# Kernel optimization log

Measured on AMD Instinct MI355X. Metric: run time of the kernel, lower is better.

Reference implementation:

```python
import jax, jax.numpy as jnp
import numpy as np

WIN = (8, 7, 7)
SHIFT = (4, 3, 3)  # window_size // 2, applied on the 2nd (shifted) block
HEADS = 24
DIM = 768
RPB_SIZE = (2 * WIN[0] - 1) * (2 * WIN[1] - 1) * (2 * WIN[2] - 1)  # 2535


def rel_pos_index():
    d, h, w = WIN
    coords = np.stack(np.meshgrid(np.arange(d), np.arange(h), np.arange(w), indexing='ij')).reshape(3, -1)
    rel = (coords[:, :, None] - coords[:, None, :]).transpose(1, 2, 0)
    rel[:, :, 0] += d - 1
    rel[:, :, 1] += h - 1
    rel[:, :, 2] += w - 1
    rel[:, :, 0] *= (2 * h - 1) * (2 * w - 1)
    rel[:, :, 1] *= 2 * w - 1
    return rel.sum(-1).astype(np.int32)


def compute_mask(D, H, W):
    # static shapes -> pure numpy, traced-constant under jit
    img = np.zeros((D, H, W), np.float32)
    cnt = 0
    sl = lambda ws, ss: [slice(None, -ws), slice(-ws, -ss), slice(-ss, None)]
    for d in sl(WIN[0], SHIFT[0]):
        for h in sl(WIN[1], SHIFT[1]):
            for w in sl(WIN[2], SHIFT[2]):
                img[d, h, w] = cnt
                cnt += 1
    m = img.reshape(D // WIN[0], WIN[0], H // WIN[1], WIN[1], W // WIN[2], WIN[2])
    m = m.transpose(0, 2, 4, 1, 3, 5).reshape(-1, WIN[0] * WIN[1] * WIN[2])
    am = m[:, None, :] - m[:, :, None]
    return jnp.asarray(np.where(am != 0, -100.0, 0.0).astype(np.float32))  # (nW, N, N)


def window_partition(x):
    B, D, H, W, C = x.shape
    x = x.reshape(B, D // WIN[0], WIN[0], H // WIN[1], WIN[1], W // WIN[2], WIN[2], C)
    return x.transpose(0, 1, 3, 5, 2, 4, 6, 7).reshape(-1, WIN[0] * WIN[1] * WIN[2], C)


def window_reverse(win, B, D, H, W):
    x = win.reshape(B, D // WIN[0], H // WIN[1], W // WIN[2], WIN[0], WIN[1], WIN[2], -1)
    return x.transpose(0, 1, 4, 2, 5, 3, 6, 7).reshape(B, D, H, W, -1)


def layer_norm(x, g, b, eps=1e-5):
    mu = x.mean(-1, keepdims=True)
    var = ((x - mu) ** 2).mean(-1, keepdims=True)
    return (x - mu) * jax.lax.rsqrt(var + eps) * g + b


def gelu(x):
    return jax.nn.gelu(x, approximate=False)  # torch nn.GELU default = exact erf


def window_attention(xw, p, rpi, mask):
    Bw, N, C = xw.shape
    hd = C // HEADS
    qkv = (xw @ p['qkv_w'].T + p['qkv_b']).reshape(Bw, N, 3, HEADS, hd).transpose(2, 0, 3, 1, 4)
    q, k, v = qkv[0] * (hd ** -0.5), qkv[1], qkv[2]
    attn = jnp.einsum('bhnd,bhmd->bhnm', q, k)  # (Bw, H, N, N)
    bias = p['rpb'][rpi.reshape(-1)].reshape(N, N, HEADS).transpose(2, 0, 1)
    attn = attn + bias[None]
    if mask is not None:
        nW = mask.shape[0]
        attn = (attn.reshape(Bw // nW, nW, HEADS, N, N) + mask[None, :, None]).reshape(Bw, HEADS, N, N)
    attn = jax.nn.softmax(attn, axis=-1)
    out = jnp.einsum('bhnm,bhmd->bhnd', attn, v).transpose(0, 2, 1, 3).reshape(Bw, N, C)
    return out @ p['proj_w'].T + p['proj_b']


def swin_block(x, p, shifted, mask, rpi):
    B, D, H, W, C = x.shape
    shortcut = x
    h = layer_norm(x, p['n1_g'], p['n1_b'])
    if shifted:
        h = jnp.roll(h, (-SHIFT[0], -SHIFT[1], -SHIFT[2]), axis=(1, 2, 3))
    w = window_attention(window_partition(h), p, rpi, mask if shifted else None)
    h = window_reverse(w, B, D, H, W)
    if shifted:
        h = jnp.roll(h, SHIFT, axis=(1, 2, 3))
    x = shortcut + h
    h = layer_norm(x, p['n2_g'], p['n2_b'])
    h = gelu(h @ p['fc1_w'].T + p['fc1_b']) @ p['fc2_w'].T + p['fc2_b']
    return x + h


def _forward(x, n1_g, n1_b, qkv_w, qkv_b, proj_w, proj_b, rpb, n2_g, n2_b, fc1_w, fc1_b, fc2_w, fc2_b, hln_g, hln_b, c1_w, c1_b, c2_w, c2_b, rpi):
    B, C, D, H, W = x.shape
    mask = compute_mask(D, H, W)
    blk = dict(n1_g=n1_g, n1_b=n1_b, qkv_w=qkv_w, qkv_b=qkv_b, proj_w=proj_w, proj_b=proj_b, rpb=rpb,
               n2_g=n2_g, n2_b=n2_b, fc1_w=fc1_w, fc1_b=fc1_b, fc2_w=fc2_w, fc2_b=fc2_b)
    outs = []
    for br in range(2):  # batch1 (score) / batch2 (weight) branches
        h = x.transpose(0, 2, 3, 4, 1)  # b c d h w -> b d h w c
        for bl in range(2):  # depth=2; second block is shifted
            p = {k: v[br, bl] for k, v in blk.items()}
            h = swin_block(h, p, bl % 2 == 1, mask, rpi)
        y = layer_norm(h, hln_g[br], hln_b[br])          # nn.LayerNorm(768)
        y = gelu(jnp.einsum('bdhwc,oc->bdhwo', y, c1_w[br]) + c1_b[br])  # Conv3d 768->64 k=1 + GELU
        y = gelu(jnp.einsum('bdhwo,po->bdhwp', y, c2_w[br]) + c2_b[br])  # Conv3d 64->2 k=1 + GELU
        outs.append(y)
    return (outs[0] * outs[1]).transpose(0, 4, 1, 2, 3)  # score * weight -> (B, 2, D, H, W)


def setup_inputs():
    key = jax.random.key(0)
    ks = jax.random.split(key, 8)
    B, T, Hs, Ws = 2, 16, 14, 14
    s = 0.02
    f = lambda i, shape: jax.random.normal(ks[i], shape, jnp.float32) * s
    return dict(
        x=jax.random.normal(ks[0], (B, DIM, T, Hs, Ws), jnp.float32),
        n1_g=jnp.ones((2, 2, DIM), jnp.float32), n1_b=jnp.zeros((2, 2, DIM), jnp.float32),
        qkv_w=f(1, (2, 2, 3 * DIM, DIM)), qkv_b=jnp.zeros((2, 2, 3 * DIM), jnp.float32),
        proj_w=f(2, (2, 2, DIM, DIM)), proj_b=jnp.zeros((2, 2, DIM), jnp.float32),
        rpb=f(3, (2, 2, RPB_SIZE, HEADS)),
        n2_g=jnp.ones((2, 2, DIM), jnp.float32), n2_b=jnp.zeros((2, 2, DIM), jnp.float32),
        fc1_w=f(4, (2, 2, 4 * DIM, DIM)), fc1_b=jnp.zeros((2, 2, 4 * DIM), jnp.float32),
        fc2_w=f(5, (2, 2, DIM, 4 * DIM)), fc2_b=jnp.zeros((2, 2, DIM), jnp.float32),
        hln_g=jnp.ones((2, DIM), jnp.float32), hln_b=jnp.zeros((2, DIM), jnp.float32),
        c1_w=f(6, (2, 64, DIM)), c1_b=jnp.zeros((2, 64), jnp.float32),
        c2_w=f(7, (2, 2, 64)), c2_b=jnp.zeros((2, 2), jnp.float32),
        rpi=jnp.asarray(rel_pos_index()),
    )


def reference(x, n1_g, n1_b, qkv_w, qkv_b, proj_w, proj_b, rpb, n2_g, n2_b, fc1_w, fc1_b, fc2_w, fc2_b, hln_g, hln_b, c1_w, c1_b, c2_w, c2_b, rpi):
    return _forward(x, n1_g, n1_b, qkv_w, qkv_b, proj_w, proj_b, rpb, n2_g, n2_b, fc1_w, fc1_b, fc2_w, fc2_b, hln_g, hln_b, c1_w, c1_b, c2_w, c2_b, rpi)
```

## Files before the change

kernel.cpp:

```cpp
#include <hip/hip_runtime.h>
#include <hip/hip_bf16.h>

#define T_TOK 6272
#define CDIM  768
#define NTOK  392
#define NWIN  16
#define NHEADS 24
#define HDIM  32
#define QSCALE 0.17677669529663687f

#define NKT 26
#define NQT 25
#define KS_ST 40
#define VS_ST 456
#define PS_ST 424

typedef unsigned short ushort_t;
typedef __attribute__((ext_vector_type(8))) short bf16x8;
typedef __attribute__((ext_vector_type(4))) short bf16x4;
typedef __attribute__((ext_vector_type(4))) float f32x4;

__device__ __forceinline__ float bf2f(ushort_t h) {
    union { unsigned int u; float f; } v; v.u = ((unsigned int)h) << 16; return v.f;
}
__device__ __forceinline__ ushort_t f2bf(float f) {
    return __bfloat16_as_ushort(__float2bfloat16(f));
}
__device__ __forceinline__ float gelu_f(float x) {
    return 0.5f * x * (1.0f + erff(x * 0.70710678118654752f));
}

__device__ __forceinline__ void gload16(const ushort_t* g, ushort_t* l) {
    __builtin_amdgcn_global_load_lds(
        (const __attribute__((address_space(1))) void*)g,
        (__attribute__((address_space(3))) void*)l,
        16, 0, 0);
}

__global__ __launch_bounds__(256) void k_transpose_in(const float* __restrict__ x,
                                                      float* __restrict__ X) {
    __shared__ float tile[32][33];
    int b  = blockIdx.z;
    int s0 = blockIdx.x * 32, c0 = blockIdx.y * 32;
    int tx = threadIdx.x, ty = threadIdx.y;
#pragma unroll
    for (int r = 0; r < 4; ++r)
        tile[ty + r * 8][tx] = x[((size_t)b * 768 + c0 + ty + r * 8) * 3136 + s0 + tx];
    __syncthreads();
#pragma unroll
    for (int r = 0; r < 4; ++r)
        X[((size_t)b * 3136 + s0 + ty + r * 8) * 768 + c0 + tx] = tile[tx][ty + r * 8];
}

__global__ __launch_bounds__(256) void k_f2b(const float* __restrict__ s,
                                             ushort_t* __restrict__ d, int n4) {
    int i = blockIdx.x * 256 + threadIdx.x;
    if (i >= n4) return;
    float4 v = ((const float4*)s)[i];
    bf16x4 r;
    r[0] = (short)f2bf(v.x); r[1] = (short)f2bf(v.y);
    r[2] = (short)f2bf(v.z); r[3] = (short)f2bf(v.w);
    *(bf16x4*)&d[(size_t)i * 4] = r;
}

__global__ __launch_bounds__(256) void k_rpbT(const float* __restrict__ rpb,
                                              float* __restrict__ rpbT) {
    int idx = blockIdx.x * 256 + threadIdx.x;
    if (idx >= 24 * 2535) return;
    int h = idx / 2535, r = idx - h * 2535;
    rpbT[idx] = rpb[(size_t)r * 24 + h];
}

__global__ __launch_bounds__(256) void k_bias(const float* __restrict__ rpbT,
                                              const int* __restrict__ rpi,
                                              ushort_t* __restrict__ Bias) {
    int row = blockIdx.x;
    int h = row / 392, i = row - h * 392;
    const float* rp = rpbT + (size_t)h * 2535;
    const int* ri = rpi + (size_t)i * NTOK;
    ushort_t* out = Bias + (size_t)row * 416;
    for (int j = threadIdx.x; j < 416; j += 256) {
        float v = (j < NTOK) ? rp[ri[j]] : 0.f;
        out[j] = f2bf(v);
    }
}

__global__ __launch_bounds__(256) void k_ln_bf(const float* __restrict__ X,
                                               ushort_t* __restrict__ Y,
                                               const float* __restrict__ g,
                                               const float* __restrict__ bta,
                                               int mode) {
    int row = blockIdx.x;
    int src = row;
    if (mode != 0) {
        int wi = row / NTOK, n = row % NTOK;
        int b = wi >> 3, rem = wi & 7;
        int wd = rem >> 2, wh = (rem >> 1) & 1, ww = rem & 1;
        int dn = n / 49, r2 = n % 49, hn = r2 / 7, wn = r2 % 7;
        int d = wd * 8 + dn, h = wh * 7 + hn, w = ww * 7 + wn;
        if (mode == 2) { d = (d + 4) & 15; h = (h + 3) % 14; w = (w + 3) % 14; }
        src = (b * 16 + d) * 196 + h * 14 + w;
    }
    const float* xr = X + (size_t)src * CDIM;
    int tid = threadIdx.x;
    float v0 = xr[tid], v1 = xr[tid + 256], v2 = xr[tid + 512];
    float s = v0 + v1 + v2;
    float q = v0 * v0 + v1 * v1 + v2 * v2;
    __shared__ float red[8];
#pragma unroll
    for (int off = 32; off > 0; off >>= 1) {
        s += __shfl_down(s, off);
        q += __shfl_down(q, off);
    }
    int lane = tid & 63, wv = tid >> 6;
    if (lane == 0) { red[wv] = s; red[4 + wv] = q; }
    __syncthreads();
    float ts = red[0] + red[1] + red[2] + red[3];
    float tq = red[4] + red[5] + red[6] + red[7];
    float mu  = ts * (1.0f / 768.0f);
    float var = tq * (1.0f / 768.0f) - mu * mu;
    float rstd = rsqrtf(var + 1e-5f);
    ushort_t* yr = Y + (size_t)row * CDIM;
    yr[tid]       = f2bf((v0 - mu) * rstd * g[tid]       + bta[tid]);
    yr[tid + 256] = f2bf((v1 - mu) * rstd * g[tid + 256] + bta[tid + 256]);
    yr[tid + 512] = f2bf((v2 - mu) * rstd * g[tid + 512] + bta[tid + 512]);
}

__global__ __launch_bounds__(256) void k_ln_f32(const float* __restrict__ X,
                                                float* __restrict__ Y,
                                                const float* __restrict__ g,
                                                const float* __restrict__ bta) {
    int row = blockIdx.x, tid = threadIdx.x;
    const float* xr = X + (size_t)row * CDIM;
    float v0 = xr[tid], v1 = xr[tid + 256], v2 = xr[tid + 512];
    float s = v0 + v1 + v2;
    float q = v0 * v0 + v1 * v1 + v2 * v2;
    __shared__ float red[8];
#pragma unroll
    for (int off = 32; off > 0; off >>= 1) {
        s += __shfl_down(s, off);
        q += __shfl_down(q, off);
    }
    int lane = tid & 63, wv = tid >> 6;
    if (lane == 0) { red[wv] = s; red[4 + wv] = q; }
    __syncthreads();
    float ts = red[0] + red[1] + red[2] + red[3];
    float tq = red[4] + red[5] + red[6] + red[7];
    float mu  = ts * (1.0f / 768.0f);
    float var = tq * (1.0f / 768.0f) - mu * mu;
    float rstd = rsqrtf(var + 1e-5f);
    float* yr = Y + (size_t)row * CDIM;
    yr[tid]       = (v0 - mu) * rstd * g[tid]       + bta[tid];
    yr[tid + 256] = (v1 - mu) * rstd * g[tid + 256] + bta[tid + 256];
    yr[tid + 512] = (v2 - mu) * rstd * g[tid + 512] + bta[tid + 512];
}

__global__ __launch_bounds__(256) void k_gemm_mfma(const ushort_t* __restrict__ A,
                                                   const ushort_t* __restrict__ W,
                                                   const float* __restrict__ bias,
                                                   float* __restrict__ Cf,
                                                   ushort_t* __restrict__ Cb,
                                                   int M, int N, int K,
                                                   int act, int remap, int accum, int outbf) {
    __shared__ ushort_t As[128 * 32];
    __shared__ ushort_t Bs[128 * 32];
    int tid = threadIdx.x, lane = tid & 63, w = tid >> 6;
    int wm = w >> 1, wn = w & 1;
    int m0 = blockIdx.y * 128, n0 = blockIdx.x * 128;

    int rr = lane >> 2, ss = (lane & 3) * 8;
    const ushort_t* gA0 = A + (size_t)(m0 + w * 32 + rr) * K + ss;
    const ushort_t* gA1 = gA0 + (size_t)16 * K;
    const ushort_t* gB0 = W + (size_t)(n0 + w * 32 + rr) * K + ss;
    const ushort_t* gB1 = gB0 + (size_t)16 * K;
    ushort_t* lA0 = &As[(w * 32) * 32];
    ushort_t* lA1 = lA0 + 512;
    ushort_t* lB0 = &Bs[(w * 32) * 32];
    ushort_t* lB1 = lB0 + 512;

    f32x4 acc[4][4];
#pragma unroll
    for (int mi = 0; mi < 4; ++mi)
#pragma unroll
        for (int ni = 0; ni < 4; ++ni) acc[mi][ni] = (f32x4){0.f, 0.f, 0.f, 0.f};

    for (int k0 = 0; k0 < K; k0 += 32) {
        __syncthreads();
        gload16(gA0 + k0, lA0);
        gload16(gA1 + k0, lA1);
        gload16(gB0 + k0, lB0);
        gload16(gB1 + k0, lB1);
        __syncthreads();
        bf16x8 af[4], bg[4];
#pragma unroll
        for (int mi = 0; mi < 4; ++mi)
            af[mi] = *(const bf16x8*)&As[(wm * 64 + mi * 16 + (lane & 15)) * 32 + (lane >> 4) * 8];
#pragma unroll
        for (int ni = 0; ni < 4; ++ni)
            bg[ni] = *(const bf16x8*)&Bs[(wn * 64 + ni * 16 + (lane & 15)) * 32 + (lane >> 4) * 8];
#pragma unroll
        for (int mi = 0; mi < 4; ++mi)
#pragma unroll
            for (int ni = 0; ni < 4; ++ni)
                acc[mi][ni] = __builtin_amdgcn_mfma_f32_16x16x32_bf16(af[mi], bg[ni], acc[mi][ni], 0, 0, 0);
    }

    int cl = lane & 15, rq = lane >> 4;
#pragma unroll
    for (int mi = 0; mi < 4; ++mi) {
#pragma unroll
        for (int ni = 0; ni < 4; ++ni) {
            int gcol = n0 + wn * 64 + ni * 16 + cl;
            float bv = bias[gcol];
#pragma unroll
            for (int i = 0; i < 4; ++i) {
                int r = m0 + wm * 64 + mi * 16 + rq * 4 + i;
                float v = acc[mi][ni][i] + bv;
                if (act) v = gelu_f(v);
                if (outbf) {
                    float sc = (outbf == 2 && gcol < 768) ? QSCALE : 1.0f;
                    Cb[(size_t)r * N + gcol] = f2bf(v * sc);
                } else {
                    size_t orow;
                    if (remap == 0) {
                        orow = (size_t)r * N;
                    } else {
                        int wi = r / NTOK, n = r % NTOK;
                        int b = wi >> 3, rem = wi & 7;
                        int wd = rem >> 2, wh = (rem >> 1) & 1, ww = rem & 1;
                        int dn = n / 49, r2 = n % 49, hn = r2 / 7, wnn = r2 % 7;
                        int d = wd * 8 + dn, h = wh * 7 + hn, ww2 = ww * 7 + wnn;
                        if (remap == 2) { d = (d + 4) & 15; h = (h + 3) % 14; ww2 = (ww2 + 3) % 14; }
                        orow = (size_t)((b * 16 + d) * 196 + h * 14 + ww2) * N;
                    }
                    if (accum) Cf[orow + gcol] += v;
                    else       Cf[orow + gcol] = v;
                }
            }
        }
    }
}

__global__ __launch_bounds__(256) void k_gemm_f32(const float* __restrict__ A,
                                                  const float* __restrict__ W,
                                                  const float* __restrict__ bias,
                                                  float* __restrict__ C,
                                                  int M, int N, int K, int act) {
    __shared__ float As[16][64];
    __shared__ float Bs[16][64];
    int tid = threadIdx.x;
    int m0 = blockIdx.y * 64, n0 = blockIdx.x * 64;
    int lrow = tid >> 2;
    int lk   = (tid & 3) * 4;
    const float* aptr = A + (size_t)(m0 + lrow) * K + lk;
    const float* wptr = W + (size_t)(n0 + lrow) * K + lk;
    int tx = tid & 15, ty = tid >> 4;
    float acc[4][4] = {};
    for (int kt = 0; kt < K; kt += 16) {
        float4 av = *(const float4*)(aptr + kt);
        float4 wv4 = *(const float4*)(wptr + kt);
        As[lk + 0][lrow] = av.x;  As[lk + 1][lrow] = av.y;
        As[lk + 2][lrow] = av.z;  As[lk + 3][lrow] = av.w;
        Bs[lk + 0][lrow] = wv4.x; Bs[lk + 1][lrow] = wv4.y;
        Bs[lk + 2][lrow] = wv4.z; Bs[lk + 3][lrow] = wv4.w;
        __syncthreads();
#pragma unroll
        for (int k = 0; k < 16; ++k) {
            float4 a = *(const float4*)&As[k][ty * 4];
            float4 b = *(const float4*)&Bs[k][tx * 4];
            float avv[4] = {a.x, a.y, a.z, a.w};
            float bvv[4] = {b.x, b.y, b.z, b.w};
#pragma unroll
            for (int i = 0; i < 4; ++i)
#pragma unroll
                for (int j = 0; j < 4; ++j)
                    acc[i][j] += avv[i] * bvv[j];
        }
        __syncthreads();
    }
    float bvals[4];
#pragma unroll
    for (int j = 0; j < 4; ++j) bvals[j] = bias[n0 + tx * 4 + j];
#pragma unroll
    for (int i = 0; i < 4; ++i) {
        int r = m0 + ty * 4 + i;
#pragma unroll
        for (int j = 0; j < 4; ++j) {
            float v = acc[i][j] + bvals[j];
            if (act) v = gelu_f(v);
            C[(size_t)r * N + n0 + tx * 4 + j] = v;
        }
    }
}

__global__ __launch_bounds__(256) void k_attn_mfma(const ushort_t* __restrict__ QKVb,
                                                   const ushort_t* __restrict__ Bias,
                                                   ushort_t* __restrict__ AO,
                                                   int shifted) {
    __shared__ int      Lrid[NTOK];
    __shared__ ushort_t Ks[NTOK * KS_ST];
    __shared__ ushort_t Vs[32 * VS_ST];
    __shared__ ushort_t Ps[4][16 * PS_ST];

    int wi   = blockIdx.x / NHEADS;
    int head = blockIdx.x % NHEADS;
    int wbase = wi * NTOK;
    int tid = threadIdx.x, lane = tid & 63, wv = tid >> 6;
    int cl = lane & 15, g = lane >> 4;
    const ushort_t* QW = QKVb + (size_t)wbase * 2304;

    for (int idx = tid; idx < NTOK * 4; idx += 256) {
        int j = idx >> 2, d8 = (idx & 3) * 8;
        const ushort_t* rowp = QW + (size_t)j * 2304 + head * 32 + d8;
        bf16x8 kv = *(const bf16x8*)(rowp + 768);
        *(bf16x8*)&Ks[j * KS_ST + d8] = kv;
        bf16x8 vv = *(const bf16x8*)(rowp + 1536);
#pragma unroll
        for (int t = 0; t < 8; ++t)
            Vs[(d8 + t) * VS_ST + j] = (ushort_t)vv[t];
    }
    for (int idx = tid; idx < 32 * 24; idx += 256) {
        int d = idx / 24, jj = idx - d * 24;
        Vs[d * VS_ST + 392 + jj] = 0;
    }
    if (shifted) {
        int rem = wi & 7;
        int wd = rem >> 2, wh = (rem >> 1) & 1, ww = rem & 1;
        for (int idx = tid; idx < NTOK; idx += 256) {
            int dn = idx / 49, r2 = idx % 49, hn = r2 / 7, wn = r2 % 7;
            int d = wd * 8 + dn, h = wh * 7 + hn, w = ww * 7 + wn;
            Lrid[idx] = (((d < 8) ? 0 : (d < 12 ? 1 : 2)) * 3 +
                         ((h < 7) ? 0 : (h < 11 ? 1 : 2))) * 3 +
                         ((w < 7) ? 0 : (w < 11 ? 1 : 2));
        }
    }
    __syncthreads();

    ushort_t* Pw = Ps[wv];
    const ushort_t* Bh = Bias + (size_t)head * 392 * 416;

    for (int qt = wv; qt < NQT; qt += 4) {
        int qrow = qt * 16 + cl; if (qrow > 391) qrow = 391;
        bf16x8 qfrag = *(const bf16x8*)(QW + (size_t)qrow * 2304 + head * 32 + g * 8);

        f32x4 acc[NKT];
#pragma unroll
        for (int kt = 0; kt < NKT; ++kt) {
            int krow = kt * 16 + cl; if (krow > 391) krow = 391;
            bf16x8 kfrag = *(const bf16x8*)&Ks[krow * KS_ST + g * 8];
            acc[kt] = __builtin_amdgcn_mfma_f32_16x16x32_bf16(
                qfrag, kfrag, (f32x4){0.f, 0.f, 0.f, 0.f}, 0, 0, 0);
        }

        int qc[4], ridq[4];
        float mrow[4];
#pragma unroll
        for (int i = 0; i < 4; ++i) {
            int qg = qt * 16 + g * 4 + i;
            qc[i] = qg > 391 ? 391 : qg;
            ridq[i] = shifted ? Lrid[qc[i]] : 0;
            mrow[i] = -1e30f;
        }
#pragma unroll
        for (int kt = 0; kt < NKT; ++kt) {
            int key = kt * 16 + cl;
            int kc = key > 391 ? 391 : key;
            int ridk = shifted ? Lrid[kc] : 0;
            bool pad = key > 391;
#pragma unroll
            for (int i = 0; i < 4; ++i) {
                float s = acc[kt][i] + bf2f(Bh[(size_t)qc[i] * 416 + key]);
                if (shifted && ridk != ridq[i]) s -= 100.0f;
                if (pad) s = -1e30f;
                acc[kt][i] = s;
                mrow[i] = fmaxf(mrow[i], s);
            }
        }
#pragma unroll
        for (int off = 1; off < 16; off <<= 1)
#pragma unroll
            for (int i = 0; i < 4; ++i)
                mrow[i] = fmaxf(mrow[i], __shfl_xor(mrow[i], off));

        float srow[4] = {0.f, 0.f, 0.f, 0.f};
#pragma unroll
        for (int kt = 0; kt < NKT; ++kt) {
            int key = kt * 16 + cl;
#pragma unroll
            for (int i = 0; i < 4; ++i) {
                float p = __expf(acc[kt][i] - mrow[i]);
                srow[i] += p;
                Pw[(g * 4 + i) * PS_ST + key] = f2bf(p);
            }
        }
#pragma unroll
        for (int off = 1; off < 16; off <<= 1)
#pragma unroll
            for (int i = 0; i < 4; ++i)
                srow[i] += __shfl_xor(srow[i], off);

        __threadfence_block();

        f32x4 out0 = (f32x4){0.f, 0.f, 0.f, 0.f};
        f32x4 out1 = (f32x4){0.f, 0.f, 0.f, 0.f};
#pragma unroll
        for (int c = 0; c < 13; ++c) {
            int ko = c * 32 + g * 8;
            bf16x8 pfrag = *(const bf16x8*)&Pw[cl * PS_ST + ko];
            bf16x8 v0 = *(const bf16x8*)&Vs[cl * VS_ST + ko];
            bf16x8 v1 = *(const bf16x8*)&Vs[(16 + cl) * VS_ST + ko];
            out0 = __builtin_amdgcn_mfma_f32_16x16x32_bf16(pfrag, v0, out0, 0, 0, 0);
            out1 = __builtin_amdgcn_mfma_f32_16x16x32_bf16(pfrag, v1, out1, 0, 0, 0);
        }

#pragma unroll
        for (int i = 0; i < 4; ++i) {
            float inv = 1.0f / srow[i];
            int qg = qt * 16 + g * 4 + i;
            if (qg < NTOK) {
                size_t ob = (size_t)(wbase + qg) * CDIM + head * 32;
                AO[ob + cl]      = f2bf(out0[i] * inv);
                AO[ob + 16 + cl] = f2bf(out1[i] * inv);
            }
        }
    }
}

__global__ __launch_bounds__(256) void k_head_c2(const float* __restrict__ Y64,
                                                 const float* __restrict__ w2,
                                                 const float* __restrict__ b2,
                                                 float* __restrict__ O2) {
    int idx = blockIdx.x * 256 + threadIdx.x;
    if (idx >= T_TOK * 2) return;
    int t = idx >> 1, p = idx & 1;
    const float* yr = Y64 + (size_t)t * 64;
    float acc = b2[p];
#pragma unroll
    for (int o = 0; o < 64; ++o) acc += yr[o] * w2[p * 64 + o];
    O2[idx] = gelu_f(acc);
}

__global__ __launch_bounds__(256) void k_final(const float* __restrict__ O2,
                                               float* __restrict__ out) {
    int idx = blockIdx.x * 256 + threadIdx.x;
    if (idx >= 2 * 2 * 3136) return;
    int b = idx / 6272;
    int p = (idx / 3136) & 1;
    int s = idx % 3136;
    int t = b * 3136 + s;
    out[idx] = O2[t * 2 + p] * O2[(size_t)T_TOK * 2 + t * 2 + p];
}

extern "C" void kernel_launch(void* const* d_in, const int* in_sizes, int n_in,
                              void* d_out, int out_size, void* d_ws, size_t ws_size,
                              hipStream_t stream) {
    const float* x     = (const float*)d_in[0];
    const float* n1_g  = (const float*)d_in[1];
    const float* n1_b  = (const float*)d_in[2];
    const float* qkv_w = (const float*)d_in[3];
    const float* qkv_b = (const float*)d_in[4];
    const float* proj_w= (const float*)d_in[5];
    const float* proj_b= (const float*)d_in[6];
    const float* rpb   = (const float*)d_in[7];
    const float* n2_g  = (const float*)d_in[8];
    const float* n2_b  = (const float*)d_in[9];
    const float* fc1_w = (const float*)d_in[10];
    const float* fc1_b = (const float*)d_in[11];
    const float* fc2_w = (const float*)d_in[12];
    const float* fc2_b = (const float*)d_in[13];
    const float* hln_g = (const float*)d_in[14];
    const float* hln_b = (const float*)d_in[15];
    const float* c1_w  = (const float*)d_in[16];
    const float* c1_b  = (const float*)d_in[17];
    const float* c2_w  = (const float*)d_in[18];
    const float* c2_b  = (const float*)d_in[19];
    const int*   rpi   = (const int*)d_in[20];

    float* ws   = (float*)d_ws;
    float* X    = ws;
    float* BIG  = X + (size_t)T_TOK * CDIM;
    float* Y64  = BIG + (size_t)T_TOK * 2304;
    float* O2   = Y64 + (size_t)T_TOK * 64;
    ushort_t* XWb = (ushort_t*)(O2 + 2 * T_TOK * 2);
    ushort_t* WB  = XWb + (size_t)T_TOK * CDIM;
    ushort_t* WBq = WB;
    ushort_t* WBp = WBq + (size_t)2304 * 768;
    ushort_t* WB1 = WBp + (size_t)768 * 768;
    ushort_t* WB2 = WB1 + (size_t)3072 * 768;
    ushort_t* BIGb = (ushort_t*)BIG;
    ushort_t* QKVb = (ushort_t*)BIG;
    ushort_t* BiasT = WB1;
    float* rpbT = Y64;

    const int NQ = 2304 * 768, NP = 768 * 768, N1 = 3072 * 768, N2 = 768 * 3072;

    for (int br = 0; br < 2; ++br) {
        k_transpose_in<<<dim3(98, 24, 2), dim3(32, 8), 0, stream>>>(x, X);
        for (int bl = 0; bl < 2; ++bl) {
            int pb = br * 2 + bl;
            int shifted = bl;
            k_f2b<<<(NQ / 4 + 255) / 256, 256, 0, stream>>>(qkv_w + (size_t)pb * NQ, WBq, NQ / 4);
            k_f2b<<<(NP / 4 + 255) / 256, 256, 0, stream>>>(proj_w + (size_t)pb * NP, WBp, NP / 4);

            k_rpbT<<<(24 * 2535 + 255) / 256, 256, 0, stream>>>(rpb + (size_t)pb * 2535 * 24, rpbT);
            k_bias<<<24 * 392, 256, 0, stream>>>(rpbT, rpi, BiasT);

            k_ln_bf<<<T_TOK, 256, 0, stream>>>(X, XWb, n1_g + pb * 768, n1_b + pb * 768, shifted ? 2 : 1);
            k_gemm_mfma<<<dim3(18, 49), 256, 0, stream>>>(XWb, WBq, qkv_b + pb * 2304,
                                                          (float*)0, QKVb,
                                                          T_TOK, 2304, 768, 0, 0, 0, 2);
            k_attn_mfma<<<NWIN * NHEADS, 256, 0, stream>>>(QKVb, BiasT, XWb, shifted);

            k_f2b<<<(N1 / 4 + 255) / 256, 256, 0, stream>>>(fc1_w + (size_t)pb * N1, WB1, N1 / 4);
            k_f2b<<<(N2 / 4 + 255) / 256, 256, 0, stream>>>(fc2_w + (size_t)pb * N2, WB2, N2 / 4);

            k_gemm_mfma<<<dim3(6, 49), 256, 0, stream>>>(XWb, WBp, proj_b + pb * 768,
                                                         X, (ushort_t*)0,
                                                         T_TOK, 768, 768, 0, shifted ? 2 : 1, 1, 0);
            k_ln_bf<<<T_TOK, 256, 0, stream>>>(X, XWb, n2_g + pb * 768, n2_b + pb * 768, 0);
            k_gemm_mfma<<<dim3(24, 49), 256, 0, stream>>>(XWb, WB1, fc1_b + pb * 3072,
                                                          (float*)0, BIGb,
                                                          T_TOK, 3072, 768, 1, 0, 0, 1);
            k_gemm_mfma<<<dim3(6, 49), 256, 0, stream>>>(BIGb, WB2, fc2_b + pb * 768,
                                                         X, (ushort_t*)0,
                                                         T_TOK, 768, 3072, 0, 0, 1, 0);
        }
        k_ln_f32<<<T_TOK, 256, 0, stream>>>(X, BIG, hln_g + br * 768, hln_b + br * 768);
        k_gemm_f32<<<dim3(1, 98), 256, 0, stream>>>(BIG, c1_w + (size_t)br * 64 * 768,
                                                    c1_b + br * 64, Y64,
                                                    T_TOK, 64, 768, 1);
        k_head_c2<<<(T_TOK * 2 + 255) / 256, 256, 0, stream>>>(Y64, c2_w + br * 128, c2_b + br * 2,
                                                               O2 + (size_t)br * T_TOK * 2);
    }
    k_final<<<(2 * 2 * 3136 + 255) / 256, 256, 0, stream>>>(O2, (float*)d_out);
}
```

Before: 1.912 ms.

## Double-buffer GEMM LDS tiles and swizzle workgroups across XCDs

The MFMA GEMM now keeps two LDS buffers for the A and B tiles. It prefetches the next K-slice while the current one feeds the MFMAs, which removes one barrier per iteration and overlaps global loads with compute. It also remaps the block index so that consecutive tiles land on the same XCD, with the aim of improving L2 reuse. This doubles LDS use per block, which could reduce occupancy.

```diff
diff --git a/kernel.cpp b/kernel.cpp
--- a/kernel.cpp
+++ b/kernel.cpp
@@ -162,21 +162,25 @@
                                                    ushort_t* __restrict__ Cb,
                                                    int M, int N, int K,
                                                    int act, int remap, int accum, int outbf) {
-    __shared__ ushort_t As[128 * 32];
-    __shared__ ushort_t Bs[128 * 32];
+    __shared__ ushort_t As[2][128 * 32];
+    __shared__ ushort_t Bs[2][128 * 32];
     int tid = threadIdx.x, lane = tid & 63, w = tid >> 6;
     int wm = w >> 1, wn = w & 1;
-    int m0 = blockIdx.y * 128, n0 = blockIdx.x * 128;
+
+    int nx = gridDim.x;
+    int nwg = nx * gridDim.y;
+    int orig = blockIdx.y * nx + blockIdx.x;
+    int sq = nwg >> 3, sr = nwg & 7;
+    int xcd = orig & 7, sidx = orig >> 3;
+    int swz = ((xcd < sr) ? xcd * (sq + 1) : sr * (sq + 1) + (xcd - sr) * sq) + sidx;
+    int m0 = (swz / nx) * 128, n0 = (swz % nx) * 128;
 
     int rr = lane >> 2, ss = (lane & 3) * 8;
     const ushort_t* gA0 = A + (size_t)(m0 + w * 32 + rr) * K + ss;
     const ushort_t* gA1 = gA0 + (size_t)16 * K;
     const ushort_t* gB0 = W + (size_t)(n0 + w * 32 + rr) * K + ss;
     const ushort_t* gB1 = gB0 + (size_t)16 * K;
-    ushort_t* lA0 = &As[(w * 32) * 32];
-    ushort_t* lA1 = lA0 + 512;
-    ushort_t* lB0 = &Bs[(w * 32) * 32];
-    ushort_t* lB1 = lB0 + 512;
+    int lb = (w * 32) * 32;
 
     f32x4 acc[4][4];
 #pragma unroll
@@ -184,25 +188,36 @@
 #pragma unroll
         for (int ni = 0; ni < 4; ++ni) acc[mi][ni] = (f32x4){0.f, 0.f, 0.f, 0.f};
 
-    for (int k0 = 0; k0 < K; k0 += 32) {
-        __syncthreads();
-        gload16(gA0 + k0, lA0);
-        gload16(gA1 + k0, lA1);
-        gload16(gB0 + k0, lB0);
-        gload16(gB1 + k0, lB1);
-        __syncthreads();
+    int nt = K >> 5;
+    gload16(gA0, &As[0][lb]);
+    gload16(gA1, &As[0][lb + 512]);
+    gload16(gB0, &Bs[0][lb]);
+    gload16(gB1, &Bs[0][lb + 512]);
+    __syncthreads();
+
+    int cur = 0;
+    for (int t = 0; t < nt; ++t) {
+        if (t + 1 < nt) {
+            int k1 = (t + 1) << 5;
+            gload16(gA0 + k1, &As[cur ^ 1][lb]);
+            gload16(gA1 + k1, &As[cur ^ 1][lb + 512]);
+            gload16(gB0 + k1, &Bs[cur ^ 1][lb]);
+            gload16(gB1 + k1, &Bs[cur ^ 1][lb + 512]);
+        }
         bf16x8 af[4], bg[4];
 #pragma unroll
         for (int mi = 0; mi < 4; ++mi)
-            af[mi] = *(const bf16x8*)&As[(wm * 64 + mi * 16 + (lane & 15)) * 32 + (lane >> 4) * 8];
+            af[mi] = *(const bf16x8*)&As[cur][(wm * 64 + mi * 16 + (lane & 15)) * 32 + (lane >> 4) * 8];
 #pragma unroll
         for (int ni = 0; ni < 4; ++ni)
-            bg[ni] = *(const bf16x8*)&Bs[(wn * 64 + ni * 16 + (lane & 15)) * 32 + (lane >> 4) * 8];
+            bg[ni] = *(const bf16x8*)&Bs[cur][(wn * 64 + ni * 16 + (lane & 15)) * 32 + (lane >> 4) * 8];
 #pragma unroll
         for (int mi = 0; mi < 4; ++mi)
 #pragma unroll
             for (int ni = 0; ni < 4; ++ni)
                 acc[mi][ni] = __builtin_amdgcn_mfma_f32_16x16x32_bf16(af[mi], bg[ni], acc[mi][ni], 0, 0, 0);
+        __syncthreads();
+        cur ^= 1;
     }
 
     int cl = lane & 15, rq = lane >> 4;
```

Result: slower. 1.970 ms (+3.0%).
